# Kernel optimization log

Measured on AMD Instinct MI355X. Metric: run time of the kernel, lower is better.

The kernel has to match this reference:

```python
import jax, jax.numpy as jnp
import numpy as np

B, C, S, P, R = 64, 3, 384, 32, 169  # batch, channels, img_size, patch_size, patches-per-image


def setup_inputs() -> dict:
    key = jax.random.key(0)
    k1, k2, k3 = jax.random.split(key, 3)
    x = jax.random.normal(k1, (B, C, S, S), dtype=jnp.float32)
    crop_top = jax.random.randint(k2, (B, R), 0, S - P, dtype=jnp.int32)
    crop_left = jax.random.randint(k3, (B, R), 0, S - P, dtype=jnp.int32)
    return {"x": x, "crop_top": crop_top, "crop_left": crop_left}


def _patches(x, crop_top, crop_left):
    # x: (B, C, S, S); crop_top/crop_left: (B, R) int
    Bb, Cc, Ss, _ = x.shape
    r = crop_top.shape[1]
    scale = (Ss - 1) / Ss  # align_corners=True mapping: pix = (coord+1)/2*(S-1)
    idx = jnp.arange(P, dtype=jnp.float32)
    # Original grid: grid[...,0] (x / width coord) = (i + top)/H scaled;
    #               grid[...,1] (y / height coord) = (j + left)/W scaled.
    xpix = (idx[None, None, :] + crop_top[:, :, None].astype(jnp.float32)) * scale   # (B,R,P) over output row i
    ypix = (idx[None, None, :] + crop_left[:, :, None].astype(jnp.float32)) * scale  # (B,R,P) over output col j
    x0f = jnp.floor(xpix); wx = xpix - x0f
    y0f = jnp.floor(ypix); wy = ypix - y0f
    x0 = x0f.astype(jnp.int32); x1 = jnp.minimum(x0 + 1, Ss - 1)
    y0 = y0f.astype(jnp.int32); y1 = jnp.minimum(y0 + 1, Ss - 1)

    bi = jnp.arange(Bb)[:, None, None, None, None]
    ci = jnp.arange(Cc)[None, None, :, None, None]

    def g(yi, xi):
        # out[b,r,c,i,j] = x[b, c, yi[b,r,j], xi[b,r,i]]  -> (B,R,C,P,P)
        return x[bi, ci, yi[:, :, None, None, :], xi[:, :, None, :, None]]

    wxb = wx[:, :, None, :, None]  # varies with output row i (width frac)
    wyb = wy[:, :, None, None, :]  # varies with output col j (height frac)
    out = ((1.0 - wyb) * (1.0 - wxb) * g(y0, x0)
           + (1.0 - wyb) * wxb * g(y0, x1)
           + wyb * (1.0 - wxb) * g(y1, x0)
           + wyb * wxb * g(y1, x1))
    # Rearrange 'b l c s1 s2 -> (b l) c s1 s2'  (returnGrouped=False)
    return out.reshape(Bb * r, Cc, P, P)


def reference(x, crop_top, crop_left):
    patches = _patches(x, crop_top, crop_left)
    pos = jnp.stack([crop_top, crop_left], axis=-1).astype(jnp.float32)  # (B, R, 2)
    return patches, pos
```

## Files before the change

### kernel.cpp

```cpp
#include <hip/hip_runtime.h>

#define Bn 64
#define Cn 3
#define Sn 384
#define Pn 32
#define Rn 169
#define HROWS 33
#define HPLANE (Pn * HROWS)
#define PATCH_ELEMS (Cn * Pn * Pn)
#define POS_OFFSET ((size_t)Bn * Rn * Cn * Pn * Pn)
#define NBLK (Bn * Rn)
#define SCALE (383.0f / 384.0f)

typedef float f4 __attribute__((ext_vector_type(4)));

__global__ __launch_bounds__(256) void patch_kernel(
    const float* __restrict__ x,
    const int*   __restrict__ crop_top,
    const int*   __restrict__ crop_left,
    float*       __restrict__ out)
{
    const int bid = blockIdx.x;
    const int pr  = (bid & 7) * (NBLK / 8) + (bid >> 3);
    const int b   = pr / Rn;
    const int t   = threadIdx.x;

    __shared__ float H[Cn * HPLANE];

    const int ct = crop_top[pr];
    const int cl = crop_left[pr];
    const float ctf = (float)ct, clf = (float)cl;
    const int row_base = (int)floorf(clf * SCALE);

    const int i = t & 31;
    const int g = t >> 5;
    float cx  = ((float)i + ctf) * SCALE;
    float fx  = floorf(cx);
    float wx  = cx - fx;
    float owx = 1.0f - wx;
    const float* basep = x + (size_t)b * (Cn * Sn * Sn) + (int)fx;
    const float* rp    = basep + (row_base + 4 * g) * Sn;

    float a0[Cn][4], a1[Cn][4];
    #pragma unroll
    for (int c = 0; c < Cn; ++c) {
        const float* p = rp + c * (Sn * Sn);
        #pragma unroll
        for (int k = 0; k < 4; ++k) {
            a0[c][k] = p[k * Sn];
            a1[c][k] = p[k * Sn + 1];
        }
    }
    float e0[Cn], e1[Cn];
    if (t < 32) {
        const float* p = basep + (row_base + 32) * Sn;
        #pragma unroll
        for (int c = 0; c < Cn; ++c) {
            e0[c] = p[c * (Sn * Sn)];
            e1[c] = p[c * (Sn * Sn) + 1];
        }
    }
    if (t < 2) out[POS_OFFSET + (size_t)pr * 2 + t] = (t == 0) ? ctf : clf;

    float* Hw = H + i * HROWS + 4 * g;
    #pragma unroll
    for (int c = 0; c < Cn; ++c) {
        #pragma unroll
        for (int k = 0; k < 4; ++k)
            Hw[c * HPLANE + k] = owx * a0[c][k] + wx * a1[c][k];
    }
    if (t < 32) {
        #pragma unroll
        for (int c = 0; c < Cn; ++c)
            H[c * HPLANE + t * HROWS + 32] = owx * e0[c] + wx * e1[c];
    }
    __syncthreads();

    const int jq = (t & 7) << 2;
    const int i2 = t >> 3;

    float wyv[4], owyv[4];
    int   yv[4];
    #pragma unroll
    for (int jj = 0; jj < 4; ++jj) {
        float cy = ((float)(jq + jj) + clf) * SCALE;
        float fy = floorf(cy);
        wyv[jj]  = cy - fy;
        owyv[jj] = 1.0f - wyv[jj];
        yv[jj]   = (int)fy - row_base;
    }

    float* outp = out + (size_t)pr * PATCH_ELEMS + i2 * Pn + jq;

    #pragma unroll
    for (int c = 0; c < Cn; ++c) {
        const float* Hc = H + c * HPLANE + i2 * HROWS;
        f4 v;
        #pragma unroll
        for (int jj = 0; jj < 4; ++jj) {
            float h0 = Hc[yv[jj]];
            float h1 = Hc[yv[jj] + 1];
            v[jj] = owyv[jj] * h0 + wyv[jj] * h1;
        }
        __builtin_nontemporal_store(v, (f4*)(outp + c * (Pn * Pn)));
    }
}

extern "C" void kernel_launch(void* const* d_in, const int* in_sizes, int n_in,
                              void* d_out, int out_size, void* d_ws, size_t ws_size,
                              hipStream_t stream) {
    const float* x         = (const float*)d_in[0];
    const int*   crop_top  = (const int*)d_in[1];
    const int*   crop_left = (const int*)d_in[2];
    float*       out       = (float*)d_out;

    patch_kernel<<<dim3(NBLK), dim3(256), 0, stream>>>(x, crop_top, crop_left, out);
}
```

Before: 37.48 us.

## Process two patches per block with double-buffered LDS and overlapped loads

Each block now handles two consecutive patches. The global loads for the second patch are issued before the first patch's vertical interpolation and store phase, so the load latency overlaps with that work. Two LDS buffers are used, the syncthreads calls are replaced with a lightweight LDS waitcnt plus barrier, and the launch grid is halved with per-XCD contiguous patch ranges. In exchange it raises register and LDS use per block, which can lower occupancy, and it halves the number of blocks.

```diff
diff --git a/kernel.cpp b/kernel.cpp
--- a/kernel.cpp
+++ b/kernel.cpp
@@ -7,78 +7,25 @@
 #define Rn 169
 #define HROWS 33
 #define HPLANE (Pn * HROWS)
+#define HBUF (Cn * HPLANE)
 #define PATCH_ELEMS (Cn * Pn * Pn)
 #define POS_OFFSET ((size_t)Bn * Rn * Cn * Pn * Pn)
-#define NBLK (Bn * Rn)
+#define PER_XCD 1352
 #define SCALE (383.0f / 384.0f)
+#define CSS (Cn * Sn * Sn)
 
 typedef float f4 __attribute__((ext_vector_type(4)));
 
-__global__ __launch_bounds__(256) void patch_kernel(
-    const float* __restrict__ x,
-    const int*   __restrict__ crop_top,
-    const int*   __restrict__ crop_left,
-    float*       __restrict__ out)
+__device__ __forceinline__ void lds_barrier() {
+    asm volatile("s_waitcnt lgkmcnt(0)" ::: "memory");
+    __builtin_amdgcn_s_barrier();
+    __builtin_amdgcn_sched_barrier(0);
+}
+
+__device__ __forceinline__ void phase_b(
+    const float* Hb, float* __restrict__ out, int pr, float clf, int row_base,
+    int i2, int jq)
 {
-    const int bid = blockIdx.x;
-    const int pr  = (bid & 7) * (NBLK / 8) + (bid >> 3);
-    const int b   = pr / Rn;
-    const int t   = threadIdx.x;
-
-    __shared__ float H[Cn * HPLANE];
-
-    const int ct = crop_top[pr];
-    const int cl = crop_left[pr];
-    const float ctf = (float)ct, clf = (float)cl;
-    const int row_base = (int)floorf(clf * SCALE);
-
-    const int i = t & 31;
-    const int g = t >> 5;
-    float cx  = ((float)i + ctf) * SCALE;
-    float fx  = floorf(cx);
-    float wx  = cx - fx;
-    float owx = 1.0f - wx;
-    const float* basep = x + (size_t)b * (Cn * Sn * Sn) + (int)fx;
-    const float* rp    = basep + (row_base + 4 * g) * Sn;
-
-    float a0[Cn][4], a1[Cn][4];
-    #pragma unroll
-    for (int c = 0; c < Cn; ++c) {
-        const float* p = rp + c * (Sn * Sn);
-        #pragma unroll
-        for (int k = 0; k < 4; ++k) {
-            a0[c][k] = p[k * Sn];
-            a1[c][k] = p[k * Sn + 1];
-        }
-    }
-    float e0[Cn], e1[Cn];
-    if (t < 32) {
-        const float* p = basep + (row_base + 32) * Sn;
-        #pragma unroll
-        for (int c = 0; c < Cn; ++c) {
-            e0[c] = p[c * (Sn * Sn)];
-            e1[c] = p[c * (Sn * Sn) + 1];
-        }
-    }
-    if (t < 2) out[POS_OFFSET + (size_t)pr * 2 + t] = (t == 0) ? ctf : clf;
-
-    float* Hw = H + i * HROWS + 4 * g;
-    #pragma unroll
-    for (int c = 0; c < Cn; ++c) {
-        #pragma unroll
-        for (int k = 0; k < 4; ++k)
-            Hw[c * HPLANE + k] = owx * a0[c][k] + wx * a1[c][k];
-    }
-    if (t < 32) {
-        #pragma unroll
-        for (int c = 0; c < Cn; ++c)
-            H[c * HPLANE + t * HROWS + 32] = owx * e0[c] + wx * e1[c];
-    }
-    __syncthreads();
-
-    const int jq = (t & 7) << 2;
-    const int i2 = t >> 3;
-
     float wyv[4], owyv[4];
     int   yv[4];
     #pragma unroll
@@ -89,12 +36,10 @@
         owyv[jj] = 1.0f - wyv[jj];
         yv[jj]   = (int)fy - row_base;
     }
-
     float* outp = out + (size_t)pr * PATCH_ELEMS + i2 * Pn + jq;
-
     #pragma unroll
     for (int c = 0; c < Cn; ++c) {
-        const float* Hc = H + c * HPLANE + i2 * HROWS;
+        const float* Hc = Hb + c * HPLANE + i2 * HROWS;
         f4 v;
         #pragma unroll
         for (int jj = 0; jj < 4; ++jj) {
@@ -106,6 +51,123 @@
     }
 }
 
+__global__ __launch_bounds__(256) void patch_kernel(
+    const float* __restrict__ x,
+    const int*   __restrict__ crop_top,
+    const int*   __restrict__ crop_left,
+    float*       __restrict__ out)
+{
+    __shared__ float H[2][HBUF];
+
+    const int bid = blockIdx.x;
+    const int xcd = bid & 7;
+    const int idx = bid >> 3;
+    const int pr0 = xcd * PER_XCD + idx * 2;
+    const int pr1 = pr0 + 1;
+    const int t   = threadIdx.x;
+    const int i   = t & 31;
+    const int g   = t >> 5;
+    const int jq  = (t & 7) << 2;
+    const int i2  = t >> 3;
+
+    const int ct0 = crop_top[pr0], cl0 = crop_left[pr0];
+    const int ct1 = crop_top[pr1], cl1 = crop_left[pr1];
+    const float ctf0 = (float)ct0, clf0 = (float)cl0;
+    const float ctf1 = (float)ct1, clf1 = (float)cl1;
+    const int rb0 = (int)floorf(clf0 * SCALE);
+    const int rb1 = (int)floorf(clf1 * SCALE);
+    const int b0 = pr0 / Rn, b1 = pr1 / Rn;
+
+    {
+        float cx  = ((float)i + ctf0) * SCALE;
+        float fx  = floorf(cx);
+        float wx  = cx - fx, owx = 1.0f - wx;
+        const float* basep = x + (size_t)b0 * CSS + (int)fx;
+        const float* rp    = basep + (rb0 + 4 * g) * Sn;
+        float a0[Cn][4], a1[Cn][4];
+        #pragma unroll
+        for (int c = 0; c < Cn; ++c) {
+            const float* p = rp + c * (Sn * Sn);
+            #pragma unroll
+            for (int k = 0; k < 4; ++k) {
+                a0[c][k] = p[k * Sn];
+                a1[c][k] = p[k * Sn + 1];
+            }
+        }
+        float e0[Cn], e1[Cn];
+        if (t < 32) {
+            const float* p = basep + (rb0 + 32) * Sn;
+            #pragma unroll
+            for (int c = 0; c < Cn; ++c) {
+                e0[c] = p[c * (Sn * Sn)];
+                e1[c] = p[c * (Sn * Sn) + 1];
+            }
+        }
+        float* Hw = H[0] + i * HROWS + 4 * g;
+        #pragma unroll
+        for (int c = 0; c < Cn; ++c)
+            #pragma unroll
+            for (int k = 0; k < 4; ++k)
+                Hw[c * HPLANE + k] = owx * a0[c][k] + wx * a1[c][k];
+        if (t < 32) {
+            #pragma unroll
+            for (int c = 0; c < Cn; ++c)
+                H[0][c * HPLANE + t * HROWS + 32] = owx * e0[c] + wx * e1[c];
+        }
+    }
+
+    float cx1  = ((float)i + ctf1) * SCALE;
+    float fx1  = floorf(cx1);
+    float wx1  = cx1 - fx1, owx1 = 1.0f - wx1;
+    const float* basep1 = x + (size_t)b1 * CSS + (int)fx1;
+    const float* rp1    = basep1 + (rb1 + 4 * g) * Sn;
+    float c0[Cn][4], c1[Cn][4];
+    #pragma unroll
+    for (int c = 0; c < Cn; ++c) {
+        const float* p = rp1 + c * (Sn * Sn);
+        #pragma unroll
+        for (int k = 0; k < 4; ++k) {
+            c0[c][k] = p[k * Sn];
+            c1[c][k] = p[k * Sn + 1];
+        }
+    }
+    float f0[Cn], f1[Cn];
+    if (t < 32) {
+        const float* p = basep1 + (rb1 + 32) * Sn;
+        #pragma unroll
+        for (int c = 0; c < Cn; ++c) {
+            f0[c] = p[c * (Sn * Sn)];
+            f1[c] = p[c * (Sn * Sn) + 1];
+        }
+    }
+    if (t < 2) {
+        out[POS_OFFSET + (size_t)pr0 * 2 + t] = (t == 0) ? ctf0 : clf0;
+        out[POS_OFFSET + (size_t)pr1 * 2 + t] = (t == 0) ? ctf1 : clf1;
+    }
+
+    lds_barrier();
+
+    phase_b(H[0], out, pr0, clf0, rb0, i2, jq);
+
+    {
+        float* Hw = H[1] + i * HROWS + 4 * g;
+        #pragma unroll
+        for (int c = 0; c < Cn; ++c)
+            #pragma unroll
+            for (int k = 0; k < 4; ++k)
+                Hw[c * HPLANE + k] = owx1 * c0[c][k] + wx1 * c1[c][k];
+        if (t < 32) {
+            #pragma unroll
+            for (int c = 0; c < Cn; ++c)
+                H[1][c * HPLANE + t * HROWS + 32] = owx1 * f0[c] + wx1 * f1[c];
+        }
+    }
+
+    lds_barrier();
+
+    phase_b(H[1], out, pr1, clf1, rb1, i2, jq);
+}
+
 extern "C" void kernel_launch(void* const* d_in, const int* in_sizes, int n_in,
                               void* d_out, int out_size, void* d_ws, size_t ws_size,
                               hipStream_t stream) {
@@ -114,5 +176,6 @@
     const int*   crop_left = (const int*)d_in[2];
     float*       out       = (float*)d_out;
 
-    patch_kernel<<<dim3(NBLK), dim3(256), 0, stream>>>(x, crop_top, crop_left, out);
+    patch_kernel<<<dim3(8 * (PER_XCD / 2)), dim3(256), 0, stream>>>(
+        x, crop_top, crop_left, out);
 }
```

New measurement: 37.95 us. No clear change (+1.3%).
